# Kernel tuning notes

Hardware: AMD Instinct MI355X
Metric: run time of the kernel (lower is better)

## Reference

```python
import jax, jax.numpy as jnp
import numpy as np

EPS = 1e-5

def layer_norm(x, g, b):
    mu = jnp.mean(x, axis=-1, keepdims=True)
    var = jnp.mean(jnp.square(x - mu), axis=-1, keepdims=True)
    return (x - mu) * jax.lax.rsqrt(var + EPS) * g + b

def setup_inputs() -> dict:
    B, T, C, H = 8, 1024, 1024, 16
    hs = C // H
    key = jax.random.key(0)
    ks = jax.random.split(key, 12)
    s = 0.02
    return {
        "x": jax.random.normal(ks[0], (B, T, C), dtype=jnp.float32),
        # per-head projections, stacked: [H, C, hs]
        "wq": jax.random.normal(ks[1], (H, C, hs), dtype=jnp.float32) * s,
        "wk": jax.random.normal(ks[2], (H, C, hs), dtype=jnp.float32) * s,
        "wv": jax.random.normal(ks[3], (H, C, hs), dtype=jnp.float32) * s,
        "w_proj": jax.random.normal(ks[4], (C, C), dtype=jnp.float32) * s,
        "b_proj": jnp.zeros((C,), dtype=jnp.float32),
        "ln1_g": jnp.ones((C,), dtype=jnp.float32),
        "ln1_b": jnp.zeros((C,), dtype=jnp.float32),
        "ln2_g": jnp.ones((C,), dtype=jnp.float32),
        "ln2_b": jnp.zeros((C,), dtype=jnp.float32),
        "w1": jax.random.normal(ks[5], (C, 4 * C), dtype=jnp.float32) * s,
        "b1": jnp.zeros((4 * C,), dtype=jnp.float32),
        "w2": jax.random.normal(ks[6], (4 * C, C), dtype=jnp.float32) * s,
        "b2": jnp.zeros((C,), dtype=jnp.float32),
    }

def reference(x, wq, wk, wv, w_proj, b_proj, ln1_g, ln1_b, ln2_g, ln2_b, w1, b1, w2, b2):
    B, T, C = x.shape
    # --- self-attention (pre-norm) ---
    h = layer_norm(x, ln1_g, ln1_b)                      # [B,T,C]
    q = jnp.einsum('btc,hcd->bhtd', h, wq)               # [B,H,T,hs]
    k = jnp.einsum('btc,hcd->bhtd', h, wk)
    v = jnp.einsum('btc,hcd->bhtd', h, wv)
    # NOTE: original scales by C**-0.5 with C = n_embed (not head_size)
    scores = jnp.einsum('bhtd,bhsd->bhts', q, k) * (C ** -0.5)
    causal = jnp.tril(jnp.ones((T, T), dtype=bool))
    scores = jnp.where(causal, scores, -jnp.inf)
    att = jax.nn.softmax(scores, axis=-1)                # dropout is identity (eval)
    out = jnp.einsum('bhts,bhsd->bhtd', att, v)          # [B,H,T,hs]
    out = out.transpose(0, 2, 1, 3).reshape(B, T, C)     # concat heads
    x = x + out @ w_proj + b_proj
    # --- feed-forward (pre-norm) ---
    h2 = layer_norm(x, ln2_g, ln2_b)
    x = x + jax.nn.relu(h2 @ w1 + b1) @ w2 + b2
    return x
```

## Files before the change

### kernel.cpp

```cpp
#include <hip/hip_runtime.h>
#include <cstdint>

typedef __attribute__((ext_vector_type(8))) __bf16 bf16x8;
typedef __attribute__((ext_vector_type(4))) float f32x4;

__device__ __forceinline__ unsigned short f2bf(float f) {
  union { float f; unsigned int u; } v; v.f = f;
  unsigned int u = v.u;
  return (unsigned short)((u + 0x7FFFu + ((u >> 16) & 1u)) >> 16);
}

__device__ __forceinline__ void load_lds16(const unsigned short* g, unsigned short* l) {
  __builtin_amdgcn_global_load_lds(
      (const __attribute__((address_space(1))) unsigned int*)g,
      (__attribute__((address_space(3))) unsigned int*)l, 16, 0, 0);
}

__global__ void transpose_all(const float* __restrict__ wq, const float* __restrict__ wk,
                              const float* __restrict__ wv, const float* __restrict__ w_proj,
                              const float* __restrict__ w1, const float* __restrict__ w2,
                              unsigned short* __restrict__ qkvt, unsigned short* __restrict__ projt,
                              unsigned short* __restrict__ w1t, unsigned short* __restrict__ w2t) {
  __shared__ float tile[32][33];
  const int id = blockIdx.x;
  const float* src;
  unsigned short* dst;
  int K, N, nt, kt;
  if (id < 3072) {
    const int which = id >> 10, rem = id & 1023;
    const int slice = rem >> 6, t = rem & 63;
    src = (which == 0 ? wq : which == 1 ? wk : wv) + (long)slice * 65536;
    dst = qkvt + (long)which * 1048576 + (long)slice * 65536;
    K = 1024; N = 64;
    nt = (t & 1) * 32; kt = (t >> 1) * 32;
  } else if (id < 4096) {
    const int t = id - 3072;
    src = w_proj; dst = projt; K = 1024; N = 1024;
    nt = (t & 31) * 32; kt = (t >> 5) * 32;
  } else if (id < 8192) {
    const int t = id - 4096;
    src = w1; dst = w1t; K = 1024; N = 4096;
    nt = (t & 127) * 32; kt = (t >> 7) * 32;
  } else {
    const int t = id - 8192;
    src = w2; dst = w2t; K = 4096; N = 1024;
    nt = (t & 31) * 32; kt = (t >> 5) * 32;
  }
  const int tx = threadIdx.x & 31, ty = threadIdx.x >> 5;
#pragma unroll
  for (int i = 0; i < 4; i++)
    tile[ty + 8 * i][tx] = src[(long)(kt + ty + 8 * i) * N + nt + tx];
  __syncthreads();
#pragma unroll
  for (int i = 0; i < 4; i++)
    dst[(long)(nt + ty + 8 * i) * K + kt + tx] = f2bf(tile[tx][ty + 8 * i]);
}

__global__ __launch_bounds__(256, 4) void ln_kernel(const float* __restrict__ x,
                                                    const float* __restrict__ g,
                                                    const float* __restrict__ b,
                                                    unsigned short* __restrict__ out) {
  const int row = blockIdx.x, tid = threadIdx.x;
  const int wave = tid >> 6, lane = tid & 63;
  const float4 xv = *(const float4*)&x[(long)row * 1024 + tid * 4];
  float s1 = xv.x + xv.y + xv.z + xv.w;
  float s2 = xv.x * xv.x + xv.y * xv.y + xv.z * xv.z + xv.w * xv.w;
#pragma unroll
  for (int m = 1; m < 64; m <<= 1) { s1 += __shfl_xor(s1, m); s2 += __shfl_xor(s2, m); }
  __shared__ float a1[4], a2[4];
  if (lane == 0) { a1[wave] = s1; a2[wave] = s2; }
  __syncthreads();
  s1 = a1[0] + a1[1] + a1[2] + a1[3];
  s2 = a2[0] + a2[1] + a2[2] + a2[3];
  const float mu = s1 * (1.f / 1024.f);
  const float var = s2 * (1.f / 1024.f) - mu * mu;
  const float rs = rsqrtf(var + 1e-5f);
  const float4 gv = *(const float4*)&g[tid * 4];
  const float4 bv = *(const float4*)&b[tid * 4];
  ushort4 o;
  o.x = f2bf((xv.x - mu) * rs * gv.x + bv.x);
  o.y = f2bf((xv.y - mu) * rs * gv.y + bv.y);
  o.z = f2bf((xv.z - mu) * rs * gv.z + bv.z);
  o.w = f2bf((xv.w - mu) * rs * gv.w + bv.w);
  *(ushort4*)&out[(long)row * 1024 + tid * 4] = o;
}

#define EPI_QKV 0
#define EPI_F32 1
#define EPI_RELU 2

template <int EPI>
__global__ __launch_bounds__(256, 3) void gemm_bt(
    const unsigned short* __restrict__ A, const unsigned short* __restrict__ Bt,
    int M, int N, int K,
    const float* __restrict__ bias, const float* __restrict__ resid,
    float* __restrict__ outF, unsigned short* __restrict__ outB,
    unsigned short* __restrict__ qb, unsigned short* __restrict__ kb,
    unsigned short* __restrict__ vTb) {
  __shared__ __attribute__((aligned(16))) unsigned short Alds[128 * 64];
  __shared__ __attribute__((aligned(16))) unsigned short Blds[128 * 64];
  const int tid = threadIdx.x;
  const int wave = tid >> 6, lane = tid & 63;
  const int quad = lane >> 4, l15 = lane & 15;
  const long tM = (long)blockIdx.x * 128;
  const long tN = (long)blockIdx.y * 128;
  const int wm = (wave >> 1) * 64, wn = (wave & 1) * 64;

  const unsigned short* aP[4];
  const unsigned short* bP[4];
  unsigned short* lA[4];
  unsigned short* lB[4];
#pragma unroll
  for (int qq = 0; qq < 4; qq++) {
    int p = (qq * 4 + wave) * 64 + lane;
    int m = p >> 3;
    int kc = (p & 7) ^ (m & 7);
    aP[qq] = A + (tM + m) * K + kc * 8;
    bP[qq] = Bt + (tN + m) * K + kc * 8;
    lA[qq] = Alds + (qq * 4 + wave) * 512;
    lB[qq] = Blds + (qq * 4 + wave) * 512;
  }

  f32x4 acc[4][4];
#pragma unroll
  for (int i = 0; i < 4; i++)
#pragma unroll
    for (int j = 0; j < 4; j++) acc[i][j] = (f32x4){0.f, 0.f, 0.f, 0.f};

  for (int k0 = 0; k0 < K; k0 += 64) {
    __syncthreads();
#pragma unroll
    for (int qq = 0; qq < 4; qq++) {
      load_lds16(aP[qq], lA[qq]);
      load_lds16(bP[qq], lB[qq]);
      aP[qq] += 64;
      bP[qq] += 64;
    }
    __syncthreads();
#pragma unroll
    for (int ks = 0; ks < 2; ks++) {
      bf16x8 af[4], bfr[4];
#pragma unroll
      for (int mt = 0; mt < 4; mt++) {
        int ml = wm + mt * 16 + l15;
        int pc = (ks * 4 + quad) ^ (ml & 7);
        af[mt] = *(const bf16x8*)&Alds[(ml * 8 + pc) * 8];
      }
#pragma unroll
      for (int nt = 0; nt < 4; nt++) {
        int nl = wn + nt * 16 + l15;
        int pc = (ks * 4 + quad) ^ (nl & 7);
        bfr[nt] = *(const bf16x8*)&Blds[(nl * 8 + pc) * 8];
      }
#pragma unroll
      for (int mt = 0; mt < 4; mt++)
#pragma unroll
        for (int nt = 0; nt < 4; nt++)
          acc[mt][nt] = __builtin_amdgcn_mfma_f32_16x16x32_bf16(af[mt], bfr[nt], acc[mt][nt], 0, 0, 0);
    }
  }

#pragma unroll
  for (int mt = 0; mt < 4; mt++) {
#pragma unroll
    for (int nt = 0; nt < 4; nt++) {
      const long col = tN + wn + nt * 16 + l15;
      const long row0 = tM + wm + mt * 16 + quad * 4;
      if (EPI == EPI_F32) {
        const float bv = bias[col];
#pragma unroll
        for (int r = 0; r < 4; r++) {
          long idx = (row0 + r) * N + col;
          outF[idx] = acc[mt][nt][r] + bv + resid[idx];
        }
      } else if (EPI == EPI_RELU) {
        const float bv = bias[col];
#pragma unroll
        for (int r = 0; r < 4; r++) {
          float v = acc[mt][nt][r] + bv;
          outB[(row0 + r) * N + col] = f2bf(v > 0.f ? v : 0.f);
        }
      } else {
        const int which = (int)(col >> 10);
        const int hh = (int)((col >> 6) & 15);
        const int dd = (int)(col & 63);
        const int b = (int)(row0 >> 10), t0 = (int)(row0 & 1023);
        if (which == 2) {
          ushort4 pk;
          pk.x = f2bf(acc[mt][nt][0]);
          pk.y = f2bf(acc[mt][nt][1]);
          pk.z = f2bf(acc[mt][nt][2]);
          pk.w = f2bf(acc[mt][nt][3]);
          *(ushort4*)&vTb[(long)(b * 16 + hh) * 65536 + dd * 1024 + t0] = pk;
        } else {
          unsigned short* dst = (which == 0 ? qb : kb);
#pragma unroll
          for (int r = 0; r < 4; r++)
            dst[((b * 16 + hh) * 1024 + t0 + r) * 64 + dd] = f2bf(acc[mt][nt][r]);
        }
      }
    }
  }
}

__global__ __launch_bounds__(256, 4) void attn_kernel(const unsigned short* __restrict__ qb,
                                                      const unsigned short* __restrict__ kb,
                                                      const unsigned short* __restrict__ vTb,
                                                      unsigned short* __restrict__ out) {
  __shared__ __attribute__((aligned(16))) unsigned short Plds[4 * 16 * 68];
  const int bh = blockIdx.x;
  const int qt = blockIdx.y;
  const int tid = threadIdx.x;
  const int wave = tid >> 6, lane = tid & 63;
  const int quad = lane >> 4, l15 = lane & 15;

  const unsigned short* qp = qb + (long)bh * 65536;
  const unsigned short* kp = kb + (long)bh * 65536;
  const unsigned short* vp = vTb + (long)bh * 65536;

  const int qrow = qt * 64 + wave * 16 + l15;
  const bf16x8 qf0 = *(const bf16x8*)&qp[qrow * 64 + quad * 8];
  const bf16x8 qf1 = *(const bf16x8*)&qp[qrow * 64 + 32 + quad * 8];

  f32x4 O[4];
  float l_r[4] = {0.f, 0.f, 0.f, 0.f};
#pragma unroll
  for (int nt = 0; nt < 4; nt++) O[nt] = (f32x4){0.f, 0.f, 0.f, 0.f};

  unsigned short* Pl = Plds + wave * (16 * 68);
  const float cscale = 0.045084220f;
  const int tloc = wave * 16 + quad * 4;

  for (int kt = 0; kt <= qt; kt++) {
    f32x4 S[4];
#pragma unroll
    for (int nt = 0; nt < 4; nt++) {
      const unsigned short* kr = kp + (kt * 64 + nt * 16 + l15) * 64;
      bf16x8 kf0 = *(const bf16x8*)&kr[quad * 8];
      bf16x8 kf1 = *(const bf16x8*)&kr[32 + quad * 8];
      f32x4 s = (f32x4){0.f, 0.f, 0.f, 0.f};
      s = __builtin_amdgcn_mfma_f32_16x16x32_bf16(qf0, kf0, s, 0, 0, 0);
      s = __builtin_amdgcn_mfma_f32_16x16x32_bf16(qf1, kf1, s, 0, 0, 0);
      S[nt] = s;
    }

    const bool diag = (kt == qt);
#pragma unroll
    for (int nt = 0; nt < 4; nt++) {
      const int sg = nt * 16 + l15;
#pragma unroll
      for (int r = 0; r < 4; r++) {
        float pv = exp2f(S[nt][r] * cscale);
        if (diag && sg > tloc + r) pv = 0.f;
        l_r[r] += pv;
        Pl[(quad * 4 + r) * 68 + sg] = f2bf(pv);
      }
    }
    __threadfence_block();

#pragma unroll
    for (int ks2 = 0; ks2 < 2; ks2++) {
      bf16x8 pa = *(const bf16x8*)&Pl[l15 * 68 + ks2 * 32 + quad * 8];
#pragma unroll
      for (int nt = 0; nt < 4; nt++) {
        bf16x8 vf = *(const bf16x8*)&vp[(nt * 16 + l15) * 1024 + kt * 64 + ks2 * 32 + quad * 8];
        O[nt] = __builtin_amdgcn_mfma_f32_16x16x32_bf16(pa, vf, O[nt], 0, 0, 0);
      }
    }
  }

#pragma unroll
  for (int r = 0; r < 4; r++) {
    l_r[r] += __shfl_xor(l_r[r], 1);
    l_r[r] += __shfl_xor(l_r[r], 2);
    l_r[r] += __shfl_xor(l_r[r], 4);
    l_r[r] += __shfl_xor(l_r[r], 8);
    l_r[r] = __builtin_amdgcn_rcpf(l_r[r]);
  }

  const int b = bh >> 4, h = bh & 15;
#pragma unroll
  for (int nt = 0; nt < 4; nt++) {
#pragma unroll
    for (int r = 0; r < 4; r++) {
      const int t = qt * 64 + wave * 16 + quad * 4 + r;
      out[(long)(b * 1024 + t) * 1024 + h * 64 + nt * 16 + l15] = f2bf(O[nt][r] * l_r[r]);
    }
  }
}

extern "C" void kernel_launch(void* const* d_in, const int* in_sizes, int n_in,
                              void* d_out, int out_size, void* d_ws, size_t ws_size,
                              hipStream_t stream) {
  const float* x = (const float*)d_in[0];
  const float* wq = (const float*)d_in[1];
  const float* wk = (const float*)d_in[2];
  const float* wv = (const float*)d_in[3];
  const float* w_proj = (const float*)d_in[4];
  const float* b_proj = (const float*)d_in[5];
  const float* ln1_g = (const float*)d_in[6];
  const float* ln1_b = (const float*)d_in[7];
  const float* ln2_g = (const float*)d_in[8];
  const float* ln2_b = (const float*)d_in[9];
  const float* w1 = (const float*)d_in[10];
  const float* b1 = (const float*)d_in[11];
  const float* w2 = (const float*)d_in[12];
  const float* b2 = (const float*)d_in[13];
  float* out = (float*)d_out;

  char* w = (char*)d_ws;
  unsigned short* h1 = (unsigned short*)w;      w += (size_t)8192 * 1024 * 2;
  unsigned short* wqkvt = (unsigned short*)w;   w += (size_t)3072 * 1024 * 2;
  unsigned short* wprojt = (unsigned short*)w;  w += (size_t)1024 * 1024 * 2;
  unsigned short* w1t = (unsigned short*)w;     w += (size_t)4096 * 1024 * 2;
  unsigned short* w2t = (unsigned short*)w;     w += (size_t)4096 * 1024 * 2;
  unsigned short* qbuf = (unsigned short*)w;    w += (size_t)128 * 1024 * 64 * 2;
  unsigned short* kbuf = (unsigned short*)w;    w += (size_t)128 * 1024 * 64 * 2;
  unsigned short* vTbuf = (unsigned short*)w;   w += (size_t)128 * 1024 * 64 * 2;
  unsigned short* act = (unsigned short*)w;     w += (size_t)8192 * 4096 * 2;
  unsigned short* attnO = h1;
  unsigned short* h2 = qbuf;

  transpose_all<<<12288, 256, 0, stream>>>(wq, wk, wv, w_proj, w1, w2,
                                           wqkvt, wprojt, w1t, w2t);

  ln_kernel<<<8192, 256, 0, stream>>>(x, ln1_g, ln1_b, h1);

  gemm_bt<EPI_QKV><<<dim3(64, 24), 256, 0, stream>>>(h1, wqkvt, 8192, 3072, 1024,
                                                     nullptr, nullptr, nullptr, nullptr,
                                                     qbuf, kbuf, vTbuf);

  attn_kernel<<<dim3(128, 16), 256, 0, stream>>>(qbuf, kbuf, vTbuf, attnO);

  gemm_bt<EPI_F32><<<dim3(64, 8), 256, 0, stream>>>(attnO, wprojt, 8192, 1024, 1024,
                                                    b_proj, x, out, nullptr,
                                                    nullptr, nullptr, nullptr);

  ln_kernel<<<8192, 256, 0, stream>>>(out, ln2_g, ln2_b, h2);

  gemm_bt<EPI_RELU><<<dim3(64, 32), 256, 0, stream>>>(h2, w1t, 8192, 4096, 1024,
                                                      b1, nullptr, nullptr, act,
                                                      nullptr, nullptr, nullptr);

  gemm_bt<EPI_F32><<<dim3(64, 8), 256, 0, stream>>>(act, w2t, 8192, 1024, 4096,
                                                    b2, out, out, nullptr,
                                                    nullptr, nullptr, nullptr);
}
```

Measured before the change: 521.2 us.

## Stage K/V tiles in swizzled LDS and process 128 query rows per block

The attention kernel now loads each 64-key K and V^T tile into LDS once per block via global_load_lds with an XOR swizzle, instead of every wave reading K/V from global memory directly. Each block now covers 128 query rows (two 16-row groups per wave), which halves the grid and doubles K/V reuse per load. Groups entirely above the causal diagonal skip their tile. The cost is two __syncthreads per key tile, more registers for the doubled accumulators, and fewer blocks, which may lower occupancy and worsen load balance.

```diff
diff --git a/kernel.cpp b/kernel.cpp
--- a/kernel.cpp
+++ b/kernel.cpp
@@ -207,9 +207,11 @@
                                                       const unsigned short* __restrict__ kb,
                                                       const unsigned short* __restrict__ vTb,
                                                       unsigned short* __restrict__ out) {
+  __shared__ __attribute__((aligned(16))) unsigned short Klds[64 * 64];
+  __shared__ __attribute__((aligned(16))) unsigned short Vlds[64 * 64];
   __shared__ __attribute__((aligned(16))) unsigned short Plds[4 * 16 * 68];
   const int bh = blockIdx.x;
-  const int qt = blockIdx.y;
+  const int qt2 = blockIdx.y;
   const int tid = threadIdx.x;
   const int wave = tid >> 6, lane = tid & 63;
   const int quad = lane >> 4, l15 = lane & 15;
@@ -218,73 +220,105 @@
   const unsigned short* kp = kb + (long)bh * 65536;
   const unsigned short* vp = vTb + (long)bh * 65536;
 
-  const int qrow = qt * 64 + wave * 16 + l15;
-  const bf16x8 qf0 = *(const bf16x8*)&qp[qrow * 64 + quad * 8];
-  const bf16x8 qf1 = *(const bf16x8*)&qp[qrow * 64 + 32 + quad * 8];
-
-  f32x4 O[4];
-  float l_r[4] = {0.f, 0.f, 0.f, 0.f};
-#pragma unroll
-  for (int nt = 0; nt < 4; nt++) O[nt] = (f32x4){0.f, 0.f, 0.f, 0.f};
+  bf16x8 qf[2][2];
+#pragma unroll
+  for (int g = 0; g < 2; g++) {
+    const int qrow = qt2 * 128 + (wave * 2 + g) * 16 + l15;
+    qf[g][0] = *(const bf16x8*)&qp[qrow * 64 + quad * 8];
+    qf[g][1] = *(const bf16x8*)&qp[qrow * 64 + 32 + quad * 8];
+  }
+
+  f32x4 O[2][4];
+  float l_r[2][4];
+#pragma unroll
+  for (int g = 0; g < 2; g++) {
+#pragma unroll
+    for (int nt = 0; nt < 4; nt++) O[g][nt] = (f32x4){0.f, 0.f, 0.f, 0.f};
+#pragma unroll
+    for (int r = 0; r < 4; r++) l_r[g][r] = 0.f;
+  }
 
   unsigned short* Pl = Plds + wave * (16 * 68);
   const float cscale = 0.045084220f;
-  const int tloc = wave * 16 + quad * 4;
-
-  for (int kt = 0; kt <= qt; kt++) {
-    f32x4 S[4];
-#pragma unroll
-    for (int nt = 0; nt < 4; nt++) {
-      const unsigned short* kr = kp + (kt * 64 + nt * 16 + l15) * 64;
-      bf16x8 kf0 = *(const bf16x8*)&kr[quad * 8];
-      bf16x8 kf1 = *(const bf16x8*)&kr[32 + quad * 8];
-      f32x4 s = (f32x4){0.f, 0.f, 0.f, 0.f};
-      s = __builtin_amdgcn_mfma_f32_16x16x32_bf16(qf0, kf0, s, 0, 0, 0);
-      s = __builtin_amdgcn_mfma_f32_16x16x32_bf16(qf1, kf1, s, 0, 0, 0);
-      S[nt] = s;
-    }
-
-    const bool diag = (kt == qt);
-#pragma unroll
-    for (int nt = 0; nt < 4; nt++) {
-      const int sg = nt * 16 + l15;
-#pragma unroll
-      for (int r = 0; r < 4; r++) {
-        float pv = exp2f(S[nt][r] * cscale);
-        if (diag && sg > tloc + r) pv = 0.f;
-        l_r[r] += pv;
-        Pl[(quad * 4 + r) * 68 + sg] = f2bf(pv);
-      }
-    }
-    __threadfence_block();
-
-#pragma unroll
-    for (int ks2 = 0; ks2 < 2; ks2++) {
-      bf16x8 pa = *(const bf16x8*)&Pl[l15 * 68 + ks2 * 32 + quad * 8];
+  const int kmax = 2 * qt2 + 1;
+
+  for (int kt = 0; kt <= kmax; kt++) {
+    __syncthreads();
+#pragma unroll
+    for (int c = 0; c < 2; c++) {
+      const int pb = (wave * 2 + c) * 64;
+      const int p = pb + lane;
+      const int m = p >> 3;
+      const int kc = (p & 7) ^ (m & 7);
+      load_lds16(kp + (kt * 64 + m) * 64 + kc * 8, Klds + pb * 8);
+      load_lds16(vp + m * 1024 + kt * 64 + kc * 8, Vlds + pb * 8);
+    }
+    __syncthreads();
+
+#pragma unroll
+    for (int g = 0; g < 2; g++) {
+      const int rowbase = qt2 * 128 + (wave * 2 + g) * 16;
+      if (kt * 64 >= rowbase + 16) continue;
+
+      f32x4 S[4];
 #pragma unroll
       for (int nt = 0; nt < 4; nt++) {
-        bf16x8 vf = *(const bf16x8*)&vp[(nt * 16 + l15) * 1024 + kt * 64 + ks2 * 32 + quad * 8];
-        O[nt] = __builtin_amdgcn_mfma_f32_16x16x32_bf16(pa, vf, O[nt], 0, 0, 0);
-      }
-    }
-  }
-
-#pragma unroll
-  for (int r = 0; r < 4; r++) {
-    l_r[r] += __shfl_xor(l_r[r], 1);
-    l_r[r] += __shfl_xor(l_r[r], 2);
-    l_r[r] += __shfl_xor(l_r[r], 4);
-    l_r[r] += __shfl_xor(l_r[r], 8);
-    l_r[r] = __builtin_amdgcn_rcpf(l_r[r]);
+        const int row = nt * 16 + l15;
+        const int pc0 = quad ^ (row & 7);
+        const int pc1 = (quad + 4) ^ (row & 7);
+        bf16x8 kf0 = *(const bf16x8*)&Klds[(row * 8 + pc0) * 8];
+        bf16x8 kf1 = *(const bf16x8*)&Klds[(row * 8 + pc1) * 8];
+        f32x4 s = (f32x4){0.f, 0.f, 0.f, 0.f};
+        s = __builtin_amdgcn_mfma_f32_16x16x32_bf16(qf[g][0], kf0, s, 0, 0, 0);
+        s = __builtin_amdgcn_mfma_f32_16x16x32_bf16(qf[g][1], kf1, s, 0, 0, 0);
+        S[nt] = s;
+      }
+
+      const bool diag = (kt * 64 + 63 > rowbase);
+      const int tb = rowbase + quad * 4;
+#pragma unroll
+      for (int nt = 0; nt < 4; nt++) {
+        const int sg = kt * 64 + nt * 16 + l15;
+#pragma unroll
+        for (int r = 0; r < 4; r++) {
+          float pv = exp2f(S[nt][r] * cscale);
+          if (diag && sg > tb + r) pv = 0.f;
+          l_r[g][r] += pv;
+          Pl[(quad * 4 + r) * 68 + nt * 16 + l15] = f2bf(pv);
+        }
+      }
+      __threadfence_block();
+
+#pragma unroll
+      for (int ks2 = 0; ks2 < 2; ks2++) {
+        bf16x8 pa = *(const bf16x8*)&Pl[l15 * 68 + ks2 * 32 + quad * 8];
+#pragma unroll
+        for (int nt = 0; nt < 4; nt++) {
+          const int d = nt * 16 + l15;
+          const int pc = (ks2 * 4 + quad) ^ (d & 7);
+          bf16x8 vf = *(const bf16x8*)&Vlds[(d * 8 + pc) * 8];
+          O[g][nt] = __builtin_amdgcn_mfma_f32_16x16x32_bf16(pa, vf, O[g][nt], 0, 0, 0);
+        }
+      }
+      __threadfence_block();
+    }
   }
 
   const int b = bh >> 4, h = bh & 15;
 #pragma unroll
-  for (int nt = 0; nt < 4; nt++) {
+  for (int g = 0; g < 2; g++) {
 #pragma unroll
     for (int r = 0; r < 4; r++) {
-      const int t = qt * 64 + wave * 16 + quad * 4 + r;
-      out[(long)(b * 1024 + t) * 1024 + h * 64 + nt * 16 + l15] = f2bf(O[nt][r] * l_r[r]);
+      float lv = l_r[g][r];
+      lv += __shfl_xor(lv, 1);
+      lv += __shfl_xor(lv, 2);
+      lv += __shfl_xor(lv, 4);
+      lv += __shfl_xor(lv, 8);
+      lv = __builtin_amdgcn_rcpf(lv);
+      const int t = qt2 * 128 + (wave * 2 + g) * 16 + quad * 4 + r;
+#pragma unroll
+      for (int nt = 0; nt < 4; nt++)
+        out[(long)(b * 1024 + t) * 1024 + h * 64 + nt * 16 + l15] = f2bf(O[g][nt][r] * lv);
     }
   }
 }
@@ -330,7 +364,7 @@
                                                      nullptr, nullptr, nullptr, nullptr,
                                                      qbuf, kbuf, vTbuf);
 
-  attn_kernel<<<dim3(128, 16), 256, 0, stream>>>(qbuf, kbuf, vTbuf, attnO);
+  attn_kernel<<<dim3(128, 8), 256, 0, stream>>>(qbuf, kbuf, vTbuf, attnO);
 
   gemm_bt<EPI_F32><<<dim3(64, 8), 256, 0, stream>>>(attnO, wprojt, 8192, 1024, 1024,
                                                     b_proj, x, out, nullptr,
```

New measurement: 449.9 us. -13.7%, faster.
